# Optimization experiments

Measured on AMD Instinct MI355X. Metric: run time of the kernel, lower is better.

The kernel has to match this reference:

```python
import jax, jax.numpy as jnp
import numpy as np

N = 100000   # nodes
E = 1600000  # edges
D = 64       # in_channel == out_channel
NEG_SLOPE = 0.01  # nn.LeakyReLU default


def gcn_conv(x, W, b, src, dst, n):
    # PyG GCNConv: add self-loops, sym-normalize by in-degree (at col/dst),
    # norm(e) = deg[src]^-1/2 * deg[dst]^-1/2, aggregate at dst, then + bias.
    deg = jnp.zeros((n,), x.dtype).at[dst].add(1.0) + 1.0  # in-degree incl. self-loop
    dinv = jax.lax.rsqrt(deg)
    h = x @ W                                   # [N, Dout]
    coef = (dinv[src] * dinv[dst])[:, None]     # [E, 1]
    agg = jax.ops.segment_sum(h[src] * coef, dst, num_segments=n)  # scatter-add
    # self-loop contribution: deg[i]^-1 * h[i]
    return agg + (dinv * dinv)[:, None] * h + b


def setup_inputs() -> dict:
    key = jax.random.key(0)
    ks = jax.random.split(key, 10)
    x = jax.random.normal(ks[0], (N, D), dtype=jnp.float32)
    edge_index = jax.random.randint(ks[1], (2, E), 0, N)
    s = 1.0 / np.sqrt(D)  # glorot-ish scale
    inp = {"x": x, "edge_index": edge_index}
    for i in range(4):
        inp[f"W{i+1}"] = jax.random.normal(ks[2 + i], (D, D), dtype=jnp.float32) * s
        inp[f"b{i+1}"] = jnp.zeros((D,), dtype=jnp.float32)
    return inp


def reference(x, edge_index, W1, b1, W2, b2, W3, b3, W4, b4):
    # eval mode: F.dropout(training=False) is identity, so omitted.
    src, dst = edge_index[0], edge_index[1]
    h = x
    for W, b in ((W1, b1), (W2, b2), (W3, b3), (W4, b4)):
        h = gcn_conv(h, W, b, src, dst, N)
        h = jnp.where(h >= 0, h, NEG_SLOPE * h)  # LeakyReLU
    return h
```

## Files before the change

kernel.cpp:

```cpp
#include <hip/hip_runtime.h>
#include <hip/hip_fp16.h>

#define N_NODES 100000
#define N_EDGES 1600000
#define DIM 64
#define NEG_SLOPE 0.01f

#define BNODES 64
#define NBUCK 1563
#define BCAP 2048
#define BLOCKS1 256
#define THREADS1 1024
#define EPB (N_EDGES / BLOCKS1)

typedef _Float16 half8 __attribute__((ext_vector_type(8)));
typedef float float4v __attribute__((ext_vector_type(4)));

__global__ void prep_weights(const float* __restrict__ W0, const float* __restrict__ W1,
                             const float* __restrict__ W2, const float* __restrict__ W3,
                             __half* __restrict__ WT16) {
    const float* Ws[4] = {W0, W1, W2, W3};
    const float* W = Ws[blockIdx.x];
    __half* dst = WT16 + (size_t)blockIdx.x * DIM * DIM;
    for (int e = threadIdx.x; e < DIM * DIM; e += 256) {
        int k = e >> 6, f = e & 63;
        dst[f * DIM + k] = __float2half(W[e]);
    }
}

__global__ __launch_bounds__(THREADS1) void bucket_scatter(const int* __restrict__ src,
                                                           const int* __restrict__ dst,
                                                           int* __restrict__ gcur,
                                                           int* __restrict__ bdata) {
    __shared__ int cnt[NBUCK];
    __shared__ int cur[NBUCK];
    __shared__ int lexcl[NBUCK];
    __shared__ int base[NBUCK];
    __shared__ int scan[THREADS1];
    __shared__ int sorted_e[EPB];
    __shared__ unsigned short sorted_b[EPB];

    const int tid = threadIdx.x;
    for (int i = tid; i < NBUCK; i += THREADS1) { cnt[i] = 0; cur[i] = 0; }
    __syncthreads();

    const int e0 = blockIdx.x * EPB;
    const int e1 = e0 + EPB;

    for (int e = e0 + tid; e < e1; e += THREADS1)
        atomicAdd(&cnt[dst[e] >> 6], 1);
    __syncthreads();

    int v = 0;
    const int HALF = (NBUCK + 1) / 2;
    if (tid < HALF) {
        v = cnt[2 * tid];
        if (2 * tid + 1 < NBUCK) v += cnt[2 * tid + 1];
    }
    scan[tid] = v;
    __syncthreads();
    for (int s = 1; s < THREADS1; s <<= 1) {
        int a = (tid >= s) ? scan[tid - s] : 0;
        __syncthreads();
        scan[tid] += a;
        __syncthreads();
    }
    if (tid < HALF) {
        int ex = scan[tid] - v;
        lexcl[2 * tid] = ex;
        if (2 * tid + 1 < NBUCK) lexcl[2 * tid + 1] = ex + cnt[2 * tid];
    }

    for (int i = tid; i < NBUCK; i += THREADS1) {
        int c = cnt[i];
        base[i] = c ? atomicAdd(&gcur[i * 16], c) : 0;
    }
    __syncthreads();

    for (int e = e0 + tid; e < e1; e += THREADS1) {
        int d = dst[e];
        int b = d >> 6;
        int p = lexcl[b] + atomicAdd(&cur[b], 1);
        sorted_e[p] = src[e] | ((d & 63) << 17);
        sorted_b[p] = (unsigned short)b;
    }
    __syncthreads();

    for (int i = tid; i < EPB; i += THREADS1) {
        int b = sorted_b[i];
        bdata[(size_t)b * BCAP + base[b] + (i - lexcl[b])] = sorted_e[i];
    }
}

__global__ __launch_bounds__(256) void bucket_build(const int* __restrict__ bdata,
                                                    const int* __restrict__ gcur,
                                                    int* __restrict__ offsets,
                                                    float* __restrict__ dinv,
                                                    int* __restrict__ csr) {
    __shared__ int cnt[BNODES];
    __shared__ int excl[BNODES];
    __shared__ int part[256];
    const int tid = threadIdx.x;
    const int b = blockIdx.x;
    const int sz = gcur[b * 16];
    const int* bd = bdata + (size_t)b * BCAP;

    int s = 0;
    for (int i = tid; i < b; i += 256) s += gcur[i * 16];
    part[tid] = s;
    __syncthreads();
    for (int st = 128; st > 0; st >>= 1) {
        if (tid < st) part[tid] += part[tid + st];
        __syncthreads();
    }
    const int cbase = part[0];
    __syncthreads();

    for (int i = tid; i < BNODES; i += 256) cnt[i] = 0;
    __syncthreads();
    for (int i = tid; i < sz; i += 256)
        atomicAdd(&cnt[bd[i] >> 17], 1);
    __syncthreads();
    if (tid == 0) {
        int run = 0;
        for (int j = 0; j < BNODES; ++j) { excl[j] = run; run += cnt[j]; }
    }
    __syncthreads();

    const int nb = b * BNODES;
    for (int i = tid; i < BNODES; i += 256) {
        int n = nb + i;
        if (n < N_NODES) {
            offsets[n] = cbase + excl[i];
            dinv[n] = rsqrtf((float)(cnt[i] + 1));
        }
    }
    if (b == NBUCK - 1 && tid == 0) offsets[N_NODES] = N_EDGES;

    for (int i = tid; i < BNODES; i += 256) cnt[i] = 0;
    __syncthreads();
    for (int i = tid; i < sz; i += 256) {
        int v = bd[i];
        int l = v >> 17;
        int pos = cbase + excl[l] + atomicAdd(&cnt[l], 1);
        csr[pos] = (v & 0x1FFFF) << 6;
    }
}

__device__ __forceinline__ void stage8(__half* dst, const float* __restrict__ X, size_t off) {
    float4 f0 = *(const float4*)(X + off);
    float4 f1 = *(const float4*)(X + off + 4);
    __half2 h0 = __floats2half2_rn(f0.x, f0.y);
    __half2 h1 = __floats2half2_rn(f0.z, f0.w);
    __half2 h2 = __floats2half2_rn(f1.x, f1.y);
    __half2 h3 = __floats2half2_rn(f1.z, f1.w);
    uint4 u;
    u.x = *(unsigned int*)&h0; u.y = *(unsigned int*)&h1;
    u.z = *(unsigned int*)&h2; u.w = *(unsigned int*)&h3;
    *(uint4*)dst = u;
}
__device__ __forceinline__ void stage8(__half* dst, const __half* __restrict__ X, size_t off) {
    *(uint4*)dst = *(const uint4*)(X + off);
}

#define XPAD 72
template <typename TIN>
__global__ __launch_bounds__(256) void mm_kernel(const TIN* __restrict__ X,
                                                 const __half* __restrict__ WT,
                                                 const float* __restrict__ dinv,
                                                 __half* __restrict__ G16) {
    __shared__ __align__(16) __half xs[64][XPAD];
    __shared__ __align__(16) __half ws[64][XPAD];
    const int t = threadIdx.x;
    const int rbase = blockIdx.x * 64;

    for (int c = t; c < 512; c += 256) {
        int row = c >> 3, koff = (c & 7) * 8;
        int grow = rbase + row;
        if (grow < N_NODES) {
            stage8(&xs[row][koff], X, (size_t)grow * DIM + koff);
        } else {
            *(uint4*)&xs[row][koff] = make_uint4(0, 0, 0, 0);
        }
        stage8(&ws[row][koff], WT, (size_t)row * DIM + koff);
    }
    __syncthreads();

    const int wave = t >> 6;
    const int lane = t & 63;
    const int q = lane >> 4;
    const int c16 = lane & 15;
    const int n0 = wave * 16;

    half8 b0 = *(const half8*)&xs[n0 + c16][q * 8];
    half8 b1 = *(const half8*)&xs[n0 + c16][32 + q * 8];

    const int gnode = rbase + n0 + c16;
    float di = (gnode < N_NODES) ? dinv[gnode] : 0.f;

#pragma unroll
    for (int ft = 0; ft < 4; ++ft) {
        const int f0 = ft * 16;
        half8 a0 = *(const half8*)&ws[f0 + c16][q * 8];
        half8 a1 = *(const half8*)&ws[f0 + c16][32 + q * 8];
        float4v acc = {0.f, 0.f, 0.f, 0.f};
        acc = __builtin_amdgcn_mfma_f32_16x16x32_f16(a0, b0, acc, 0, 0, 0);
        acc = __builtin_amdgcn_mfma_f32_16x16x32_f16(a1, b1, acc, 0, 0, 0);
        if (gnode < N_NODES) {
            __half2 p0 = __floats2half2_rn(di * acc[0], di * acc[1]);
            __half2 p1 = __floats2half2_rn(di * acc[2], di * acc[3]);
            uint2 u;
            u.x = *(unsigned int*)&p0;
            u.y = *(unsigned int*)&p1;
            *(uint2*)(G16 + (size_t)gnode * DIM + f0 + q * 4) = u;
        }
    }
}

__global__ __launch_bounds__(256) void fused_agg_mm(const __half* __restrict__ Gin,
                                                    const int* __restrict__ csr,
                                                    const int* __restrict__ offsets,
                                                    const float* __restrict__ dinv,
                                                    const float* __restrict__ bias,
                                                    const __half* __restrict__ WT,
                                                    __half* __restrict__ Gout) {
    __shared__ __align__(16) __half act[64][XPAD];
    __shared__ __align__(16) __half ws[64][XPAD];
    const int t = threadIdx.x;
    const int blk = blockIdx.x;
    const int nb = blk * BNODES;

    for (int c = t; c < 512; c += 256) {
        int row = c >> 3, koff = (c & 7) * 8;
        stage8(&ws[row][koff], WT, (size_t)row * DIM + koff);
    }

    const int wave = t >> 6;
    const int lane = t & 63;
    const int grp  = lane >> 5;
    const int slot = (lane >> 3) & 3;
    const int sub  = lane & 7;
    const int fc   = sub * 8;

    for (int i = 0; i < 8; ++i) {
        const int lrow = wave * 16 + i * 2 + grp;
        const int wid = nb + lrow;
        const bool valid = (wid < N_NODES);
        const int beg = valid ? offsets[wid] : 0;
        const int end = valid ? offsets[wid + 1] : 0;

        __half2 h0 = __float2half2_rn(0.f), h1 = h0, h2 = h0, h3 = h0;

#define PKACC(vraw)                                     \
        {                                               \
            const __half2* hp = (const __half2*)&(vraw);\
            h0 = __hadd2(h0, hp[0]);                    \
            h1 = __hadd2(h1, hp[1]);                    \
            h2 = __hadd2(h2, hp[2]);                    \
            h3 = __hadd2(h3, hp[3]);                    \
        }
        int e = beg + slot;
        for (; e + 4 < end; e += 8) {
            int p0 = csr[e];
            int p1 = csr[e + 4];
            float4 v0 = *(const float4*)(Gin + (size_t)p0 + fc);
            float4 v1 = *(const float4*)(Gin + (size_t)p1 + fc);
            PKACC(v0)
            PKACC(v1)
        }
        if (e < end) {
            int p0 = csr[e];
            float4 v0 = *(const float4*)(Gin + (size_t)p0 + fc);
            PKACC(v0)
        }
#undef PKACC

        float acc[8];
        {
            float2 f;
            f = __half22float2(h0); acc[0] = f.x; acc[1] = f.y;
            f = __half22float2(h1); acc[2] = f.x; acc[3] = f.y;
            f = __half22float2(h2); acc[4] = f.x; acc[5] = f.y;
            f = __half22float2(h3); acc[6] = f.x; acc[7] = f.y;
        }
#pragma unroll
        for (int k = 0; k < 8; ++k) {
            acc[k] += __shfl_xor(acc[k], 8, 64);
            acc[k] += __shfl_xor(acc[k], 16, 64);
        }

        if (slot == 0) {
            uint4 u = make_uint4(0, 0, 0, 0);
            if (valid) {
                float4 vs = *(const float4*)(Gin + (size_t)wid * DIM + fc);
                {
                    const __half2* hp = (const __half2*)&vs;
                    float2 f0 = __half22float2(hp[0]);
                    float2 f1 = __half22float2(hp[1]);
                    float2 f2 = __half22float2(hp[2]);
                    float2 f3 = __half22float2(hp[3]);
                    acc[0] += f0.x; acc[1] += f0.y;
                    acc[2] += f1.x; acc[3] += f1.y;
                    acc[4] += f2.x; acc[5] += f2.y;
                    acc[6] += f3.x; acc[7] += f3.y;
                }
                float di = dinv[wid];
                float4 bb0 = *(const float4*)(bias + fc);
                float4 bb1 = *(const float4*)(bias + fc + 4);
                float r[8];
                r[0] = di * acc[0] + bb0.x;
                r[1] = di * acc[1] + bb0.y;
                r[2] = di * acc[2] + bb0.z;
                r[3] = di * acc[3] + bb0.w;
                r[4] = di * acc[4] + bb1.x;
                r[5] = di * acc[5] + bb1.y;
                r[6] = di * acc[6] + bb1.z;
                r[7] = di * acc[7] + bb1.w;
#pragma unroll
                for (int k = 0; k < 8; ++k)
                    r[k] = (r[k] >= 0.f) ? r[k] : NEG_SLOPE * r[k];
                __half2 q0 = __floats2half2_rn(r[0], r[1]);
                __half2 q1 = __floats2half2_rn(r[2], r[3]);
                __half2 q2 = __floats2half2_rn(r[4], r[5]);
                __half2 q3 = __floats2half2_rn(r[6], r[7]);
                u.x = *(unsigned int*)&q0;
                u.y = *(unsigned int*)&q1;
                u.z = *(unsigned int*)&q2;
                u.w = *(unsigned int*)&q3;
            }
            *(uint4*)(&act[lrow][fc]) = u;
        }
    }
    __syncthreads();

    const int q = lane >> 4;
    const int c16 = lane & 15;
    const int n0 = wave * 16;

    half8 xb0 = *(const half8*)&act[n0 + c16][q * 8];
    half8 xb1 = *(const half8*)&act[n0 + c16][32 + q * 8];

    const int gnode = nb + n0 + c16;
    float dio = (gnode < N_NODES) ? dinv[gnode] : 0.f;

#pragma unroll
    for (int ft = 0; ft < 4; ++ft) {
        const int f0 = ft * 16;
        half8 a0 = *(const half8*)&ws[f0 + c16][q * 8];
        half8 a1 = *(const half8*)&ws[f0 + c16][32 + q * 8];
        float4v accv = {0.f, 0.f, 0.f, 0.f};
        accv = __builtin_amdgcn_mfma_f32_16x16x32_f16(a0, xb0, accv, 0, 0, 0);
        accv = __builtin_amdgcn_mfma_f32_16x16x32_f16(a1, xb1, accv, 0, 0, 0);
        if (gnode < N_NODES) {
            __half2 p0 = __floats2half2_rn(dio * accv[0], dio * accv[1]);
            __half2 p1 = __floats2half2_rn(dio * accv[2], dio * accv[3]);
            uint2 u;
            u.x = *(unsigned int*)&p0;
            u.y = *(unsigned int*)&p1;
            *(uint2*)(Gout + (size_t)gnode * DIM + f0 + q * 4) = u;
        }
    }
}

#define AGG_BLOCKS 2048
#define AGG_WAVES (AGG_BLOCKS * 4)
#define NPAIRS (N_NODES / 2)
template <bool FINAL>
__global__ __launch_bounds__(256) void agg_kernel(const __half* __restrict__ G16,
                                                  const int* __restrict__ csr,
                                                  const int* __restrict__ offsets,
                                                  const float* __restrict__ dinv,
                                                  const float* __restrict__ bias,
                                                  void* __restrict__ outp) {
    const int gw = (blockIdx.x * 256 + threadIdx.x) >> 6;
    const int lane = threadIdx.x & 63;
    const int grp  = lane >> 5;
    const int slot = (lane >> 3) & 3;
    const int sub  = lane & 7;
    const int fc   = sub * 8;

    for (int p = gw; p < NPAIRS; p += AGG_WAVES) {
        const int wid = p * 2 + grp;
        const int beg = offsets[wid], end = offsets[wid + 1];

        __half2 h0 = __float2half2_rn(0.f), h1 = h0, h2 = h0, h3 = h0;

#define PKACC(vraw)                                     \
        {                                               \
            const __half2* hp = (const __half2*)&(vraw);\
            h0 = __hadd2(h0, hp[0]);                    \
            h1 = __hadd2(h1, hp[1]);                    \
            h2 = __hadd2(h2, hp[2]);                    \
            h3 = __hadd2(h3, hp[3]);                    \
        }

        int e = beg + slot;
        for (; e + 4 < end; e += 8) {
            int p0 = csr[e];
            int p1 = csr[e + 4];
            float4 v0 = *(const float4*)(G16 + (size_t)p0 + fc);
            float4 v1 = *(const float4*)(G16 + (size_t)p1 + fc);
            PKACC(v0)
            PKACC(v1)
        }
        if (e < end) {
            int p0 = csr[e];
            float4 v0 = *(const float4*)(G16 + (size_t)p0 + fc);
            PKACC(v0)
        }
#undef PKACC

        float acc[8];
        {
            float2 f;
            f = __half22float2(h0); acc[0] = f.x; acc[1] = f.y;
            f = __half22float2(h1); acc[2] = f.x; acc[3] = f.y;
            f = __half22float2(h2); acc[4] = f.x; acc[5] = f.y;
            f = __half22float2(h3); acc[6] = f.x; acc[7] = f.y;
        }
#pragma unroll
        for (int k = 0; k < 8; ++k) {
            acc[k] += __shfl_xor(acc[k], 8, 64);
            acc[k] += __shfl_xor(acc[k], 16, 64);
        }

        if (slot == 0) {
            float4 vs = *(const float4*)(G16 + (size_t)wid * DIM + fc);
            {
                const __half2* hp = (const __half2*)&vs;
                float2 f0 = __half22float2(hp[0]);
                float2 f1 = __half22float2(hp[1]);
                float2 f2 = __half22float2(hp[2]);
                float2 f3 = __half22float2(hp[3]);
                acc[0] += f0.x; acc[1] += f0.y;
                acc[2] += f1.x; acc[3] += f1.y;
                acc[4] += f2.x; acc[5] += f2.y;
                acc[6] += f3.x; acc[7] += f3.y;
            }

            float di = dinv[wid];
            float4 b0 = *(const float4*)(bias + fc);
            float4 b1 = *(const float4*)(bias + fc + 4);
            float r[8];
            r[0] = di * acc[0] + b0.x;
            r[1] = di * acc[1] + b0.y;
            r[2] = di * acc[2] + b0.z;
            r[3] = di * acc[3] + b0.w;
            r[4] = di * acc[4] + b1.x;
            r[5] = di * acc[5] + b1.y;
            r[6] = di * acc[6] + b1.z;
            r[7] = di * acc[7] + b1.w;
#pragma unroll
            for (int k = 0; k < 8; ++k)
                r[k] = (r[k] >= 0.f) ? r[k] : NEG_SLOPE * r[k];

            if (FINAL) {
                float* out = (float*)outp;
                *(float4*)(out + (size_t)wid * DIM + fc)     = make_float4(r[0], r[1], r[2], r[3]);
                *(float4*)(out + (size_t)wid * DIM + fc + 4) = make_float4(r[4], r[5], r[6], r[7]);
            } else {
                __half* act = (__half*)outp;
                __half2 q0 = __floats2half2_rn(r[0], r[1]);
                __half2 q1 = __floats2half2_rn(r[2], r[3]);
                __half2 q2 = __floats2half2_rn(r[4], r[5]);
                __half2 q3 = __floats2half2_rn(r[6], r[7]);
                uint4 u;
                u.x = *(unsigned int*)&q0;
                u.y = *(unsigned int*)&q1;
                u.z = *(unsigned int*)&q2;
                u.w = *(unsigned int*)&q3;
                *(uint4*)(act + (size_t)wid * DIM + fc) = u;
            }
        }
    }
}

extern "C" void kernel_launch(void* const* d_in, const int* in_sizes, int n_in,
                              void* d_out, int out_size, void* d_ws, size_t ws_size,
                              hipStream_t stream) {
    const float* x = (const float*)d_in[0];
    const int* ei = (const int*)d_in[1];
    const int* src = ei;
    const int* dst = ei + N_EDGES;
    const float* W[4] = {(const float*)d_in[2], (const float*)d_in[4],
                         (const float*)d_in[6], (const float*)d_in[8]};
    const float* b[4] = {(const float*)d_in[3], (const float*)d_in[5],
                         (const float*)d_in[7], (const float*)d_in[9]};
    float* out = (float*)d_out;

    char* ws = (char*)d_ws;
    size_t off = 0;
    auto alloc = [&](size_t bytes) -> void* {
        void* p = ws + off;
        off = (off + bytes + 255) & ~(size_t)255;
        return p;
    };
    __half* GA    = (__half*)alloc((size_t)N_NODES * DIM * sizeof(__half));
    __half* GB    = (__half*)alloc((size_t)N_NODES * DIM * sizeof(__half));
    __half* WT16  = (__half*)alloc((size_t)4 * DIM * DIM * sizeof(__half));
    int*   csr    = (int*)alloc((size_t)N_EDGES * sizeof(int));
    int*   bdata  = (int*)alloc((size_t)NBUCK * BCAP * sizeof(int));
    int*   gcur   = (int*)alloc((size_t)NBUCK * 16 * sizeof(int));
    int*   offsets= (int*)alloc((size_t)(N_NODES + 1) * sizeof(int));
    float* dinv   = (float*)alloc((size_t)N_NODES * sizeof(float));

    hipMemsetAsync(gcur, 0, (size_t)NBUCK * 16 * sizeof(int), stream);
    prep_weights<<<4, 256, 0, stream>>>(W[0], W[1], W[2], W[3], WT16);

    bucket_scatter<<<BLOCKS1, THREADS1, 0, stream>>>(src, dst, gcur, bdata);
    bucket_build<<<NBUCK, 256, 0, stream>>>(bdata, gcur, offsets, dinv, csr);

    const int MM_GRID = (N_NODES + 63) / 64;

    mm_kernel<float><<<MM_GRID, 256, 0, stream>>>(x, WT16, dinv, GA);
    fused_agg_mm<<<NBUCK, 256, 0, stream>>>(GA, csr, offsets, dinv, b[0], WT16 + 1 * DIM * DIM, GB);
    fused_agg_mm<<<NBUCK, 256, 0, stream>>>(GB, csr, offsets, dinv, b[1], WT16 + 2 * DIM * DIM, GA);
    fused_agg_mm<<<NBUCK, 256, 0, stream>>>(GA, csr, offsets, dinv, b[2], WT16 + 3 * DIM * DIM, GB);
    agg_kernel<true><<<AGG_BLOCKS, 256, 0, stream>>>(GB, csr, offsets, dinv, b[3], out);
}
```

Baseline: 292.4 us.

## Simplify bucket scatter to direct global writes and fold memset into prep kernel

```diff
diff --git a/kernel.cpp b/kernel.cpp
--- a/kernel.cpp
+++ b/kernel.cpp
@@ -10,7 +10,7 @@
 #define NBUCK 1563
 #define BCAP 2048
 #define BLOCKS1 256
-#define THREADS1 1024
+#define THREADS1 512
 #define EPB (N_EDGES / BLOCKS1)
 
 typedef _Float16 half8 __attribute__((ext_vector_type(8)));
@@ -18,13 +18,18 @@
 
 __global__ void prep_weights(const float* __restrict__ W0, const float* __restrict__ W1,
                              const float* __restrict__ W2, const float* __restrict__ W3,
-                             __half* __restrict__ WT16) {
-    const float* Ws[4] = {W0, W1, W2, W3};
-    const float* W = Ws[blockIdx.x];
-    __half* dst = WT16 + (size_t)blockIdx.x * DIM * DIM;
-    for (int e = threadIdx.x; e < DIM * DIM; e += 256) {
-        int k = e >> 6, f = e & 63;
-        dst[f * DIM + k] = __float2half(W[e]);
+                             __half* __restrict__ WT16, int* __restrict__ gcur) {
+    if (blockIdx.x < 4) {
+        const float* Ws[4] = {W0, W1, W2, W3};
+        const float* W = Ws[blockIdx.x];
+        __half* dst = WT16 + (size_t)blockIdx.x * DIM * DIM;
+        for (int e = threadIdx.x; e < DIM * DIM; e += 256) {
+            int k = e >> 6, f = e & 63;
+            dst[f * DIM + k] = __float2half(W[e]);
+        }
+    } else {
+        for (int i = (blockIdx.x - 4) * 256 + threadIdx.x; i < NBUCK * 16; i += 4 * 256)
+            gcur[i] = 0;
     }
 }
 
@@ -33,15 +38,10 @@
                                                            int* __restrict__ gcur,
                                                            int* __restrict__ bdata) {
     __shared__ int cnt[NBUCK];
-    __shared__ int cur[NBUCK];
-    __shared__ int lexcl[NBUCK];
     __shared__ int base[NBUCK];
-    __shared__ int scan[THREADS1];
-    __shared__ int sorted_e[EPB];
-    __shared__ unsigned short sorted_b[EPB];
 
     const int tid = threadIdx.x;
-    for (int i = tid; i < NBUCK; i += THREADS1) { cnt[i] = 0; cur[i] = 0; }
+    for (int i = tid; i < NBUCK; i += THREADS1) cnt[i] = 0;
     __syncthreads();
 
     const int e0 = blockIdx.x * EPB;
@@ -50,45 +50,19 @@
     for (int e = e0 + tid; e < e1; e += THREADS1)
         atomicAdd(&cnt[dst[e] >> 6], 1);
     __syncthreads();
-
-    int v = 0;
-    const int HALF = (NBUCK + 1) / 2;
-    if (tid < HALF) {
-        v = cnt[2 * tid];
-        if (2 * tid + 1 < NBUCK) v += cnt[2 * tid + 1];
-    }
-    scan[tid] = v;
-    __syncthreads();
-    for (int s = 1; s < THREADS1; s <<= 1) {
-        int a = (tid >= s) ? scan[tid - s] : 0;
-        __syncthreads();
-        scan[tid] += a;
-        __syncthreads();
-    }
-    if (tid < HALF) {
-        int ex = scan[tid] - v;
-        lexcl[2 * tid] = ex;
-        if (2 * tid + 1 < NBUCK) lexcl[2 * tid + 1] = ex + cnt[2 * tid];
-    }
 
     for (int i = tid; i < NBUCK; i += THREADS1) {
         int c = cnt[i];
         base[i] = c ? atomicAdd(&gcur[i * 16], c) : 0;
+        cnt[i] = 0;
     }
     __syncthreads();
 
     for (int e = e0 + tid; e < e1; e += THREADS1) {
         int d = dst[e];
         int b = d >> 6;
-        int p = lexcl[b] + atomicAdd(&cur[b], 1);
-        sorted_e[p] = src[e] | ((d & 63) << 17);
-        sorted_b[p] = (unsigned short)b;
-    }
-    __syncthreads();
-
-    for (int i = tid; i < EPB; i += THREADS1) {
-        int b = sorted_b[i];
-        bdata[(size_t)b * BCAP + base[b] + (i - lexcl[b])] = sorted_e[i];
+        int p = atomicAdd(&cnt[b], 1);
+        bdata[(size_t)b * BCAP + base[b] + p] = src[e] | ((d & 63) << 17);
     }
 }
 
@@ -504,8 +478,7 @@
     int*   offsets= (int*)alloc((size_t)(N_NODES + 1) * sizeof(int));
     float* dinv   = (float*)alloc((size_t)N_NODES * sizeof(float));
 
-    hipMemsetAsync(gcur, 0, (size_t)NBUCK * 16 * sizeof(int), stream);
-    prep_weights<<<4, 256, 0, stream>>>(W[0], W[1], W[2], W[3], WT16);
+    prep_weights<<<8, 256, 0, stream>>>(W[0], W[1], W[2], W[3], WT16, gcur);
 
     bucket_scatter<<<BLOCKS1, THREADS1, 0, stream>>>(src, dst, gcur, bdata);
     bucket_build<<<NBUCK, 256, 0, stream>>>(bdata, gcur, offsets, dinv, csr);
```

Result: no change. 294.5 us (+0.7%).
